# Kernel optimization log

Hardware: AMD Instinct MI355X
Metric: run time of the kernel (lower is better)

Reference implementation:

```python
import jax, jax.numpy as jnp
import numpy as np

H, C = 4, 32          # heads, per-head channels (hidden_dim = 128)
HID = H * C
NC, NM, E, DIN = 100000, 20000, 400000, 64


def _gat_conv(x_src, x_dst, src, dst, Wsrc, Wdst, asrc, adst, bias):
    """PyG-style bipartite GATConv: gather -> leaky-relu attention -> segment softmax -> scatter."""
    n_dst = x_dst.shape[0]
    hs = (x_src @ Wsrc).reshape(-1, H, C)            # [Ns, H, C]
    hd = (x_dst @ Wdst).reshape(-1, H, C)            # [Nd, H, C]
    a_s = jnp.sum(hs * asrc, axis=-1)                # [Ns, H]
    a_d = jnp.sum(hd * adst, axis=-1)                # [Nd, H]
    e = jax.nn.leaky_relu(a_s[src] + a_d[dst], 0.2)  # [E, H]
    m = jax.ops.segment_max(e, dst, num_segments=n_dst)
    m = jnp.where(jnp.isfinite(m), m, 0.0)           # isolated dst nodes -> -inf max
    ex = jnp.exp(e - m[dst])
    den = jax.ops.segment_sum(ex, dst, num_segments=n_dst)
    alpha = ex / (den[dst] + 1e-16)                  # per-destination segment softmax
    out = jax.ops.segment_sum(hs[src] * alpha[:, :, None], dst, num_segments=n_dst)
    return out.reshape(n_dst, HID) + bias            # concat heads + bias


def _mlp2(x, W1, b1, W2, b2):
    return jax.nn.relu(x @ W1 + b1) @ W2 + b2


def setup_inputs():
    key = jax.random.key(0)
    ks = iter(jax.random.split(key, 80))
    def rn(shape, s):
        return jax.random.normal(next(ks), shape, dtype=jnp.float32) * s
    inp = {}
    inp['x_card'] = rn((NC, DIN), 1.0)
    inp['x_merchant'] = rn((NM, DIN), 1.0)
    for l, din in ((0, DIN), (1, HID)):
        for et in ('cm', 'mc'):
            p = 'l%d_%s_' % (l, et)
            g = (2.0 / (din + HID)) ** 0.5
            inp[p + 'Wsrc'] = rn((din, HID), g)
            inp[p + 'Wdst'] = rn((din, HID), g)
            inp[p + 'asrc'] = rn((H, C), 0.1)
            inp[p + 'adst'] = rn((H, C), 0.1)
            inp[p + 'b'] = jnp.zeros((HID,), jnp.float32)
    for nt in ('card', 'merchant'):
        inp['attw_' + nt] = rn((HID, 1), 0.05)
        inp['attb_' + nt] = jnp.zeros((1,), jnp.float32)
    for nt in ('card', 'mer'):
        inp['cls_%s_W1' % nt] = rn((HID, HID // 2), 0.05)
        inp['cls_%s_b1' % nt] = jnp.zeros((HID // 2,), jnp.float32)
        inp['cls_%s_W2' % nt] = rn((HID // 2, 2), 0.05)
        inp['cls_%s_b2' % nt] = jnp.zeros((2,), jnp.float32)
    inp['risk_W1'] = rn((HID, HID // 2), 0.05)
    inp['risk_b1'] = jnp.zeros((HID // 2,), jnp.float32)
    inp['risk_W2'] = rn((HID // 2, 1), 0.05)
    inp['risk_b2'] = jnp.zeros((1,), jnp.float32)
    inp['cm_src'] = jax.random.randint(next(ks), (E,), 0, NC, dtype=jnp.int32)
    inp['cm_dst'] = jax.random.randint(next(ks), (E,), 0, NM, dtype=jnp.int32)
    inp['mc_src'] = jax.random.randint(next(ks), (E,), 0, NM, dtype=jnp.int32)
    inp['mc_dst'] = jax.random.randint(next(ks), (E,), 0, NC, dtype=jnp.int32)
    return inp


def reference(x_card, x_merchant,
              l0_cm_Wsrc, l0_cm_Wdst, l0_cm_asrc, l0_cm_adst, l0_cm_b,
              l0_mc_Wsrc, l0_mc_Wdst, l0_mc_asrc, l0_mc_adst, l0_mc_b,
              l1_cm_Wsrc, l1_cm_Wdst, l1_cm_asrc, l1_cm_adst, l1_cm_b,
              l1_mc_Wsrc, l1_mc_Wdst, l1_mc_asrc, l1_mc_adst, l1_mc_b,
              attw_card, attb_card, attw_merchant, attb_merchant,
              cls_card_W1, cls_card_b1, cls_card_W2, cls_card_b2,
              cls_mer_W1, cls_mer_b1, cls_mer_W2, cls_mer_b2,
              risk_W1, risk_b1, risk_W2, risk_b2,
              cm_src, cm_dst, mc_src, mc_dst):
    xc, xm = x_card, x_merchant
    # HeteroConv layer 0 (each dst type receives exactly one edge type, so mean-aggr is identity)
    xm1 = _gat_conv(xc, xm, cm_src, cm_dst, l0_cm_Wsrc, l0_cm_Wdst, l0_cm_asrc, l0_cm_adst, l0_cm_b)
    xc1 = _gat_conv(xm, xc, mc_src, mc_dst, l0_mc_Wsrc, l0_mc_Wdst, l0_mc_asrc, l0_mc_adst, l0_mc_b)
    # HeteroConv layer 1
    xm2 = _gat_conv(xc1, xm1, cm_src, cm_dst, l1_cm_Wsrc, l1_cm_Wdst, l1_cm_asrc, l1_cm_adst, l1_cm_b)
    xc2 = _gat_conv(xm1, xc1, mc_src, mc_dst, l1_mc_Wsrc, l1_mc_Wdst, l1_mc_asrc, l1_mc_adst, l1_mc_b)
    # graph-level attention: softmax over the node dimension (dim=0), then reweight
    xc2 = xc2 * jax.nn.softmax(xc2 @ attw_card + attb_card, axis=0)
    xm2 = xm2 * jax.nn.softmax(xm2 @ attw_merchant + attb_merchant, axis=0)
    pred_c = _mlp2(xc2, cls_card_W1, cls_card_b1, cls_card_W2, cls_card_b2)
    pred_m = _mlp2(xm2, cls_mer_W1, cls_mer_b1, cls_mer_W2, cls_mer_b2)
    risk_c = jax.nn.sigmoid(_mlp2(xc2, risk_W1, risk_b1, risk_W2, risk_b2))[:, 0]
    risk_m = jax.nn.sigmoid(_mlp2(xm2, risk_W1, risk_b1, risk_W2, risk_b2))[:, 0]
    return (xc2, xm2, pred_c, pred_m, risk_c, risk_m)
```

## Files before the change

kernel.cpp:

```cpp
#include <hip/hip_runtime.h>

typedef _Float16 f16;
typedef _Float16 f16x2 __attribute__((ext_vector_type(2)));
typedef _Float16 f16x4 __attribute__((ext_vector_type(4)));
typedef _Float16 f16x8 __attribute__((ext_vector_type(8)));
typedef float floatx4 __attribute__((ext_vector_type(4)));

constexpr int NC = 100000;
constexpr int NM = 20000;
constexpr int NE = 400000;

constexpr int OFF_XM2 = NC * 128;
constexpr int OFF_PC  = OFF_XM2 + NM * 128;
constexpr int OFF_PM  = OFF_PC + NC * 2;
constexpr int OFF_RC  = OFF_PM + NM * 2;
constexpr int OFF_RM  = OFF_RC + NC;

__device__ __forceinline__ int bpermi(int v, int srclane) {
  return __builtin_amdgcn_ds_bpermute(srclane << 2, v);
}
__device__ __forceinline__ float bpermf(float v, int srclane) {
  int r = __builtin_amdgcn_ds_bpermute(srclane << 2, __builtin_bit_cast(int, v));
  return __builtin_bit_cast(float, r);
}

__global__ void __launch_bounds__(256) k_prep(
    int* zero_base, int nzero, int* stats_i,
    const float* W0, const float* a0, float* v0,
    const float* W1, const float* a1, float* v1,
    const float* W2, const float* a2, float* v2,
    const float* W3, const float* a3, float* v3,
    const float* cb1, const float* mb1, const float* rb1, float* bC, float* bM,
    const float* S0, const float* S1, const float* S2, const float* S3,
    const float* c1, const float* m1, const float* r1,
    f16* BfL0cm, f16* BfL0mc, f16* BfL1cm, f16* BfL1mc, f16* BfC, f16* BfM) {
  int b = blockIdx.x, t = threadIdx.x;
  if (b < 256) {
    for (int i = b * 256 + t; i < nzero + 4; i += 256 * 256) {
      if (i < nzero) zero_base[i] = 0; else stats_i[i - nzero] = 0;
    }
  } else if (b == 256) {
    const float* Wd[4] = {W0, W1, W2, W3};
    const float* ad[4] = {a0, a1, a2, a3};
    float* vd[4] = {v0, v1, v2, v3};
    for (int idx = t; idx < 1536; idx += 256) {
      int mat, base;
      if (idx < 256)       { mat = 0; base = 0; }
      else if (idx < 512)  { mat = 1; base = 256; }
      else if (idx < 1024) { mat = 2; base = 512; }
      else                 { mat = 3; base = 1024; }
      int local = idx - base, k = local >> 2, h = local & 3;
      const float* W = Wd[mat]; const float* a = ad[mat];
      float s = 0.f;
      for (int c = 0; c < 32; ++c) s += W[k * 128 + h * 32 + c] * a[h * 32 + c];
      vd[mat][local] = s;
    }
    if (t < 128) {
      bC[t] = (t < 64) ? cb1[t] : rb1[t - 64];
      bM[t] = (t < 64) ? mb1[t] : rb1[t - 64];
    }
  } else {
    int s = b - 257;
    const float* Wp = nullptr; const float* cA = nullptr; const float* cB = nullptr;
    f16* dst; int kt;
    if (s < 2)       { Wp = S0; dst = BfL0cm; kt = s; }
    else if (s < 4)  { Wp = S1; dst = BfL0mc; kt = s - 2; }
    else if (s < 8)  { Wp = S2; dst = BfL1cm; kt = s - 4; }
    else if (s < 12) { Wp = S3; dst = BfL1mc; kt = s - 8; }
    else if (s < 16) { cA = c1; cB = r1; dst = BfC; kt = s - 12; }
    else             { cA = m1; cB = r1; dst = BfM; kt = s - 16; }
    for (int e = t; e < 512; e += 256) {
      int lane = e & 63, ct = e >> 6;
      int m = lane & 15, q = lane >> 4;
      int col = ct * 16 + m;
      f16x8 frag;
      #pragma unroll
      for (int j = 0; j < 8; ++j) {
        int k = kt * 32 + q * 8 + j;
        float val = Wp ? Wp[k * 128 + col]
                       : (col < 64 ? cA[k * 64 + col] : cB[k * 64 + (col - 64)]);
        frag[j] = (f16)val;
      }
      *reinterpret_cast<f16x8*>(&dst[(size_t)((kt * 8 + ct) * 64 + lane) * 8]) = frag;
    }
  }
}

__global__ void k_hist(const int* cm_dst, const int* mc_dst,
                       int* cnt_cm, int* cnt_mc, int* rank_cm, int* rank_mc) {
  int i = blockIdx.x * blockDim.x + threadIdx.x;
  if (i < NE) {
    rank_cm[i] = atomicAdd(&cnt_cm[cm_dst[i]], 1);
    rank_mc[i] = atomicAdd(&cnt_mc[mc_dst[i]], 1);
  }
}

__global__ void __launch_bounds__(256) k_scan1(const int* cnt_cm, const int* cnt_mc,
                                               int* offs_cm, int* offs_mc, int* parts) {
  int b = blockIdx.x;
  const int* cnt; int* offs; int n, chunk;
  if (b < 20) { cnt = cnt_cm; offs = offs_cm; n = NM; chunk = b; }
  else        { cnt = cnt_mc; offs = offs_mc; n = NC; chunk = b - 20; }
  int t = threadIdx.x;
  int base = chunk * 1024;
  int v[4]; int tsum = 0;
  #pragma unroll
  for (int j = 0; j < 4; ++j) {
    int idx = base + t * 4 + j;
    v[j] = (idx < n) ? cnt[idx] : 0;
    tsum += v[j];
  }
  __shared__ int sd[256];
  sd[t] = tsum; __syncthreads();
  for (int off = 1; off < 256; off <<= 1) {
    int x = (t >= off) ? sd[t - off] : 0;
    __syncthreads();
    sd[t] += x;
    __syncthreads();
  }
  int excl = sd[t] - tsum;
  int r = excl;
  #pragma unroll
  for (int j = 0; j < 4; ++j) {
    int idx = base + t * 4 + j;
    if (idx < n) offs[idx] = r;
    r += v[j];
  }
  if (t == 0) parts[b] = sd[255];
}

__global__ void __launch_bounds__(256) k_scan2(int* parts) {
  int b = blockIdx.x;
  int base = (b == 0) ? 0 : 20;
  int n = (b == 0) ? 20 : 98;
  int t = threadIdx.x;
  __shared__ int sd[128];
  int v = 0;
  if (t < 128) { v = (t < n) ? parts[base + t] : 0; sd[t] = v; }
  __syncthreads();
  for (int off = 1; off < 128; off <<= 1) {
    int x = 0;
    if (t < 128 && t >= off) x = sd[t - off];
    __syncthreads();
    if (t < 128) sd[t] += x;
    __syncthreads();
  }
  if (t < 128 && t < n) parts[base + t] = sd[t] - v;
}

__global__ void k_scan3(int* offs_cm, int* offs_mc, const int* parts) {
  int i = blockIdx.x * blockDim.x + threadIdx.x;
  if (i < NM) {
    offs_cm[i] += parts[i >> 10];
  } else if (i < NM + NC) {
    int j = i - NM;
    offs_mc[j] += parts[20 + (j >> 10)];
  }
  if (i == 0) { offs_cm[NM] = NE; offs_mc[NC] = NE; }
}

__global__ void k_scatter(const int* cm_src, const int* cm_dst,
                          const int* mc_src, const int* mc_dst,
                          const int* rank_cm, const int* rank_mc,
                          const int* offs_cm, const int* offs_mc,
                          int* csr_cm, int* csr_mc) {
  int i = blockIdx.x * blockDim.x + threadIdx.x;
  if (i < NE) {
    int p = offs_cm[cm_dst[i]] + rank_cm[i];
    csr_cm[p] = cm_src[i];
    int q = offs_mc[mc_dst[i]] + rank_mc[i];
    csr_mc[q] = mc_src[i];
  }
}

struct GemmSide {
  const float* x; const f16* Bf;
  const float* asrc; const float* v; f16* hs; float* asO; float* adO;
  const float* bias; const float* wnum; const float* den; float* outx;
  const float* W2; const float* B2; const float* w2r; const float* b2r;
  float* pred; float* risk;
  int M;
};

template<int K, int EPI>
__global__ void __launch_bounds__(256) k_gemm(GemmSide A, GemmSide B, int gridA) {
  constexpr int PP = K + 8;
  constexpr int F4 = K / 4;
  __shared__ f16 xs16[64 * PP];
  const bool isA = (int)blockIdx.x < gridA;
  GemmSide S = isA ? A : B;
  const int blk = isA ? (int)blockIdx.x : (int)blockIdx.x - gridA;
  const int rows0 = blk * 64;
  const int t = (int)threadIdx.x;
  float invden_s = 0.f;
  if constexpr (EPI == 1) invden_s = 1.0f / S.den[0];
  const float4* x4 = reinterpret_cast<const float4*>(S.x);
  #pragma unroll
  for (int ii = 0; ii < (64 * F4) / 256; ++ii) {
    int idx = t + ii * 256;
    int r = idx / F4, f = idx % F4;
    int gr = rows0 + r;
    float4 val = {0.f, 0.f, 0.f, 0.f};
    if (gr < S.M) val = x4[(size_t)gr * F4 + f];
    f16x4 hv; hv.x = (f16)val.x; hv.y = (f16)val.y; hv.z = (f16)val.z; hv.w = (f16)val.w;
    *reinterpret_cast<f16x4*>(&xs16[r * PP + f * 4]) = hv;
    if constexpr (EPI == 1) {
      if (gr < S.M) {
        float w = S.wnum[gr] * invden_s;
        float4 ov = {val.x * w, val.y * w, val.z * w, val.w * w};
        *reinterpret_cast<float4*>(&S.outx[(size_t)gr * 128 + f * 4]) = ov;
      }
    }
  }
  __syncthreads();
  const int lane = t & 63, w = t >> 6;
  const int m = lane & 15, q = lane >> 4;
  const int rbase = w * 16;
  floatx4 acc[8];
  #pragma unroll
  for (int ct = 0; ct < 8; ++ct) acc[ct] = {0.f, 0.f, 0.f, 0.f};
  const f16x8* Bf8 = reinterpret_cast<const f16x8*>(S.Bf);
  #pragma unroll
  for (int kt = 0; kt < K / 32; ++kt) {
    f16x8 a = *reinterpret_cast<const f16x8*>(&xs16[(rbase + m) * PP + kt * 32 + q * 8]);
    #pragma unroll
    for (int ct = 0; ct < 8; ++ct) {
      f16x8 b = Bf8[(kt * 8 + ct) * 64 + lane];
      acc[ct] = __builtin_amdgcn_mfma_f32_16x16x32_f16(a, b, acc[ct], 0, 0, 0);
    }
  }
  if constexpr (EPI == 0) {
    #pragma unroll
    for (int reg = 0; reg < 4; ++reg) {
      int gr = rows0 + rbase + q * 4 + reg;
      bool ok = gr < S.M;
      #pragma unroll
      for (int cp = 0; cp < 4; ++cp) {
        float v0 = acc[2 * cp][reg], v1 = acc[2 * cp + 1][reg];
        float w0 = __shfl_xor(v0, 1), w1 = __shfl_xor(v1, 1);
        bool even = (m & 1) == 0;
        f16x2 pr;
        pr.x = (f16)(even ? v0 : w1);
        pr.y = (f16)(even ? w0 : v1);
        int col = even ? (2 * cp) * 16 + m : (2 * cp + 1) * 16 + m - 1;
        if (ok) *reinterpret_cast<f16x2*>(&S.hs[(size_t)gr * 128 + col]) = pr;
      }
    }
    float as0[4], as1[4];
    #pragma unroll
    for (int h = 0; h < 4; ++h) { as0[h] = S.asrc[h * 32 + m]; as1[h] = S.asrc[h * 32 + 16 + m]; }
    #pragma unroll
    for (int reg = 0; reg < 4; ++reg) {
      float p[4];
      #pragma unroll
      for (int h = 0; h < 4; ++h)
        p[h] = acc[2 * h][reg] * as0[h] + acc[2 * h + 1][reg] * as1[h];
      #pragma unroll
      for (int off = 1; off < 16; off <<= 1) {
        #pragma unroll
        for (int h = 0; h < 4; ++h) p[h] += __shfl_xor(p[h], off);
      }
      int gr = rows0 + rbase + q * 4 + reg;
      if (m == 0 && gr < S.M) {
        float4 pv = {p[0], p[1], p[2], p[3]};
        *reinterpret_cast<float4*>(&S.asO[gr * 4]) = pv;
      }
    }
    float qd[4] = {0.f, 0.f, 0.f, 0.f};
    const float4* v4p = reinterpret_cast<const float4*>(S.v);
    constexpr int KS = K / 4;
    #pragma unroll
    for (int i = 0; i < KS; ++i) {
      int k = q * KS + i;
      float xv = (float)xs16[(rbase + m) * PP + k];
      float4 vk = v4p[k];
      qd[0] += xv * vk.x; qd[1] += xv * vk.y; qd[2] += xv * vk.z; qd[3] += xv * vk.w;
    }
    #pragma unroll
    for (int h = 0; h < 4; ++h) {
      qd[h] += __shfl_xor(qd[h], 16);
      qd[h] += __shfl_xor(qd[h], 32);
    }
    int gr2 = rows0 + rbase + m;
    if (q == 0 && gr2 < S.M) {
      float4 qv = {qd[0], qd[1], qd[2], qd[3]};
      *reinterpret_cast<float4*>(&S.adO[gr2 * 4]) = qv;
    }
  } else {
    float wn[4];
    #pragma unroll
    for (int reg = 0; reg < 4; ++reg) {
      int gr = rows0 + rbase + q * 4 + reg;
      wn[reg] = (gr < S.M) ? S.wnum[gr] * invden_s : 0.f;
    }
    float bct[8], w2c0[4], w2c1[4], w2rv[4];
    #pragma unroll
    for (int ct = 0; ct < 8; ++ct) bct[ct] = S.bias[ct * 16 + m];
    #pragma unroll
    for (int ct = 0; ct < 4; ++ct) {
      int col = ct * 16 + m;
      w2c0[ct] = S.W2[col * 2];
      w2c1[ct] = S.W2[col * 2 + 1];
      w2rv[ct] = S.w2r[col];
    }
    #pragma unroll
    for (int reg = 0; reg < 4; ++reg) {
      float p0 = 0.f, p1 = 0.f, rr = 0.f;
      #pragma unroll
      for (int ct = 0; ct < 4; ++ct) {
        float hv = fmaxf(acc[ct][reg] * wn[reg] + bct[ct], 0.f);
        p0 += hv * w2c0[ct];
        p1 += hv * w2c1[ct];
      }
      #pragma unroll
      for (int ct = 4; ct < 8; ++ct) {
        float hv = fmaxf(acc[ct][reg] * wn[reg] + bct[ct], 0.f);
        rr += hv * w2rv[ct - 4];
      }
      #pragma unroll
      for (int off = 1; off < 16; off <<= 1) {
        p0 += __shfl_xor(p0, off);
        p1 += __shfl_xor(p1, off);
        rr += __shfl_xor(rr, off);
      }
      int gr = rows0 + rbase + q * 4 + reg;
      if (m == 0 && gr < S.M) {
        float2 pp = {p0 + S.B2[0], p1 + S.B2[1]};
        *reinterpret_cast<float2*>(&S.pred[gr * 2]) = pp;
        float z = rr + S.b2r[0];
        S.risk[gr] = 1.f / (1.f + __expf(-z));
      }
    }
  }
}

struct AggSide {
  const int* offs; const int* csr; const float* as_; const float* ad;
  const f16* hs; const float* bias; float* out;
  const float* attw; const float* attb; float* logv;
};

__global__ void __launch_bounds__(256) k_agg(AggSide A, AggSide B,
                                             int ndstA, int ndstB, int nwaves) {
  const int wid = (int)blockIdx.x * 4 + ((int)threadIdx.x >> 6);
  if (wid >= nwaves) return;
  const int lane = (int)threadIdx.x & 63;
  if (wid < ndstA) {
    const AggSide S = A;
    const int d = wid;
    const int we = lane >> 2, wh = lane & 3;
    const int ep = lane >> 5;
    const int c4 = lane & 31;
    const int gh = c4 >> 3;
    const int c8 = c4 << 3;
    const int wh4 = wh << 2;
    const int beg = __builtin_amdgcn_readfirstlane(S.offs[d]);
    const int end = __builtin_amdgcn_readfirstlane(S.offs[d + 1]);
    const float adv = S.ad[d * 4 + wh];
    const char* __restrict__ hsb = (const char*)S.hs;
    const char* __restrict__ asb = (const char*)S.as_;
    float m_run = -1e30f, den = 0.f;
    float acc0 = 0.f, acc1 = 0.f, acc2 = 0.f, acc3 = 0.f;
    for (int base = beg; base < end; base += 16) {
      const int n = min(16, end - base);
      int sb = 0; float e = -1e30f;
      if (we < n) {
        int s = S.csr[base + we];
        sb = s << 8;
        float asv = *reinterpret_cast<const float*>(asb + (unsigned)((s << 4) + wh4));
        float ev = asv + adv;
        e = (ev > 0.f) ? ev : 0.2f * ev;
      }
      float cm = e;
      cm = fmaxf(cm, __shfl_xor(cm, 4));
      cm = fmaxf(cm, __shfl_xor(cm, 8));
      if (n > 4) cm = fmaxf(cm, __shfl_xor(cm, 16));
      if (n > 8) cm = fmaxf(cm, __shfl_xor(cm, 32));
      const float m_new = fmaxf(m_run, cm);
      const float scale = __expf(m_run - m_new);
      const float w = __expf(e - m_new);
      float ws = w;
      ws += __shfl_xor(ws, 4);
      ws += __shfl_xor(ws, 8);
      if (n > 4) ws += __shfl_xor(ws, 16);
      if (n > 8) ws += __shfl_xor(ws, 32);
      den = den * scale + ws;
      m_run = m_new;
      const float sg = bpermf(scale, gh);
      acc0 *= sg; acc1 *= sg; acc2 *= sg; acc3 *= sg;
      int j = 0;
      for (; j + 8 <= n; j += 8) {
        int i0 = (j + ep) << 2, i1 = (j + 2 + ep) << 2;
        int i2 = (j + 4 + ep) << 2, i3 = (j + 6 + ep) << 2;
        int s0 = bpermi(sb, i0);
        int s1 = bpermi(sb, i1);
        int s2 = bpermi(sb, i2);
        int s3 = bpermi(sb, i3);
        f16x4 h0 = *reinterpret_cast<const f16x4*>(hsb + (unsigned)(s0 + c8));
        f16x4 h1 = *reinterpret_cast<const f16x4*>(hsb + (unsigned)(s1 + c8));
        f16x4 h2 = *reinterpret_cast<const f16x4*>(hsb + (unsigned)(s2 + c8));
        f16x4 h3 = *reinterpret_cast<const f16x4*>(hsb + (unsigned)(s3 + c8));
        float w0 = bpermf(w, i0 + gh);
        float w1 = bpermf(w, i1 + gh);
        float w2 = bpermf(w, i2 + gh);
        float w3 = bpermf(w, i3 + gh);
        acc0 += w0 * (float)h0.x; acc1 += w0 * (float)h0.y;
        acc2 += w0 * (float)h0.z; acc3 += w0 * (float)h0.w;
        acc0 += w1 * (float)h1.x; acc1 += w1 * (float)h1.y;
        acc2 += w1 * (float)h1.z; acc3 += w1 * (float)h1.w;
        acc0 += w2 * (float)h2.x; acc1 += w2 * (float)h2.y;
        acc2 += w2 * (float)h2.z; acc3 += w2 * (float)h2.w;
        acc0 += w3 * (float)h3.x; acc1 += w3 * (float)h3.y;
        acc2 += w3 * (float)h3.z; acc3 += w3 * (float)h3.w;
      }
      for (; j + 4 <= n; j += 4) {
        int i0 = (j + ep) << 2, i1 = (j + 2 + ep) << 2;
        int s0 = bpermi(sb, i0);
        int s1 = bpermi(sb, i1);
        f16x4 h0 = *reinterpret_cast<const f16x4*>(hsb + (unsigned)(s0 + c8));
        f16x4 h1 = *reinterpret_cast<const f16x4*>(hsb + (unsigned)(s1 + c8));
        float w0 = bpermf(w, i0 + gh);
        float w1 = bpermf(w, i1 + gh);
        acc0 += w0 * (float)h0.x; acc1 += w0 * (float)h0.y;
        acc2 += w0 * (float)h0.z; acc3 += w0 * (float)h0.w;
        acc0 += w1 * (float)h1.x; acc1 += w1 * (float)h1.y;
        acc2 += w1 * (float)h1.z; acc3 += w1 * (float)h1.w;
      }
      for (; j < n; j += 2) {
        int i0 = (j + ep) << 2;
        int s0 = bpermi(sb, i0);
        f16x4 h0 = *reinterpret_cast<const f16x4*>(hsb + (unsigned)(s0 + c8));
        float w0 = bpermf(w, i0 + gh);
        acc0 += w0 * (float)h0.x; acc1 += w0 * (float)h0.y;
        acc2 += w0 * (float)h0.z; acc3 += w0 * (float)h0.w;
      }
    }
    acc0 += __shfl_xor(acc0, 32);
    acc1 += __shfl_xor(acc1, 32);
    acc2 += __shfl_xor(acc2, 32);
    acc3 += __shfl_xor(acc3, 32);
    const float deng = bpermf(den, gh);
    const float invden = (deng > 0.f) ? 1.f / deng : 0.f;
    const float4 b4 = *reinterpret_cast<const float4*>(&S.bias[c4 * 4]);
    float o0 = acc0 * invden + b4.x;
    float o1 = acc1 * invden + b4.y;
    float o2 = acc2 * invden + b4.z;
    float o3 = acc3 * invden + b4.w;
    if (ep == 0) {
      float4 o = {o0, o1, o2, o3};
      *reinterpret_cast<float4*>(&S.out[d * 128 + c4 * 4]) = o;
    }
    if (S.attw) {
      const float4 aw = *reinterpret_cast<const float4*>(&S.attw[c4 * 4]);
      float sl = o0 * aw.x + o1 * aw.y + o2 * aw.z + o3 * aw.w;
      sl += __shfl_xor(sl, 1);
      sl += __shfl_xor(sl, 2);
      sl += __shfl_xor(sl, 4);
      sl += __shfl_xor(sl, 8);
      sl += __shfl_xor(sl, 16);
      if (lane == 0) S.logv[d] = sl + S.attb[0];
    }
  } else {
    const AggSide S = B;
    const int p = wid - ndstA;
    const int half32 = lane & 32;
    const int l5 = lane & 31;
    int d = p * 2 + (lane >> 5);
    const bool dok = d < ndstB;
    if (!dok) d = ndstB - 1;
    const int we = l5 >> 2, wh = l5 & 3;
    const int gh = l5 >> 3;
    const int c8 = l5 << 3;
    const char* __restrict__ hsb = (const char*)S.hs;
    const char* __restrict__ asb = (const char*)S.as_;
    const int beg = S.offs[d];
    const int end = dok ? S.offs[d + 1] : beg;
    const float adv = S.ad[d * 4 + wh];
    int nch = (end - beg + 7) >> 3;
    int nco = __shfl_xor(nch, 32);
    const int ncmax = __builtin_amdgcn_readfirstlane(max(nch, nco));
    float m_run = -1e30f, den = 0.f;
    float acc0 = 0.f, acc1 = 0.f, acc2 = 0.f, acc3 = 0.f;
    for (int cc = 0; cc < ncmax; ++cc) {
      const int n = min(end - beg - cc * 8, 8);
      int sb = 0; float e = -1e30f;
      const bool wv = we < n;
      if (wv) {
        int s = S.csr[beg + cc * 8 + we];
        sb = s << 8;
        float asv = *reinterpret_cast<const float*>(asb + (unsigned)((s << 4) + (wh << 2)));
        float ev = asv + adv;
        e = (ev > 0.f) ? ev : 0.2f * ev;
      }
      float cm = e;
      cm = fmaxf(cm, __shfl_xor(cm, 4));
      cm = fmaxf(cm, __shfl_xor(cm, 8));
      cm = fmaxf(cm, __shfl_xor(cm, 16));
      const float m_new = fmaxf(m_run, cm);
      const float scale = __expf(m_run - m_new);
      const float w = wv ? __expf(e - m_new) : 0.f;
      float ws = w;
      ws += __shfl_xor(ws, 4);
      ws += __shfl_xor(ws, 8);
      ws += __shfl_xor(ws, 16);
      den = den * scale + ws;
      m_run = m_new;
      acc0 *= scale; acc1 *= scale; acc2 *= scale; acc3 *= scale;
      int jv = max(n, 0);
      int jo = __shfl_xor(jv, 32);
      const int jm = __builtin_amdgcn_readfirstlane(max(jv, jo));
      int j = 0;
      for (; j + 4 <= jm; j += 4) {
        int i0 = half32 + j * 4, i1 = i0 + 4, i2 = i0 + 8, i3 = i0 + 12;
        int s0 = bpermi(sb, i0);
        int s1 = bpermi(sb, i1);
        int s2 = bpermi(sb, i2);
        int s3 = bpermi(sb, i3);
        f16x4 h0 = *reinterpret_cast<const f16x4*>(hsb + (unsigned)(s0 + c8));
        f16x4 h1 = *reinterpret_cast<const f16x4*>(hsb + (unsigned)(s1 + c8));
        f16x4 h2 = *reinterpret_cast<const f16x4*>(hsb + (unsigned)(s2 + c8));
        f16x4 h3 = *reinterpret_cast<const f16x4*>(hsb + (unsigned)(s3 + c8));
        float w0 = bpermf(w, i0 + gh);
        float w1 = bpermf(w, i1 + gh);
        float w2 = bpermf(w, i2 + gh);
        float w3 = bpermf(w, i3 + gh);
        acc0 += w0 * (float)h0.x; acc1 += w0 * (float)h0.y;
        acc2 += w0 * (float)h0.z; acc3 += w0 * (float)h0.w;
        acc0 += w1 * (float)h1.x; acc1 += w1 * (float)h1.y;
        acc2 += w1 * (float)h1.z; acc3 += w1 * (float)h1.w;
        acc0 += w2 * (float)h2.x; acc1 += w2 * (float)h2.y;
        acc2 += w2 * (float)h2.z; acc3 += w2 * (float)h2.w;
        acc0 += w3 * (float)h3.x; acc1 += w3 * (float)h3.y;
        acc2 += w3 * (float)h3.z; acc3 += w3 * (float)h3.w;
      }
      for (; j < jm; ++j) {
        int i0 = half32 + j * 4;
        int s0 = bpermi(sb, i0);
        f16x4 h0 = *reinterpret_cast<const f16x4*>(hsb + (unsigned)(s0 + c8));
        float w0 = bpermf(w, i0 + gh);
        acc0 += w0 * (float)h0.x; acc1 += w0 * (float)h0.y;
        acc2 += w0 * (float)h0.z; acc3 += w0 * (float)h0.w;
      }
    }
    const float invden = (den > 0.f) ? 1.f / den : 0.f;
    const float4 b4 = *reinterpret_cast<const float4*>(&S.bias[l5 * 4]);
    float o0 = acc0 * invden + b4.x;
    float o1 = acc1 * invden + b4.y;
    float o2 = acc2 * invden + b4.z;
    float o3 = acc3 * invden + b4.w;
    if (dok) {
      float4 o = {o0, o1, o2, o3};
      *reinterpret_cast<float4*>(&S.out[d * 128 + l5 * 4]) = o;
    }
    if (S.attw) {
      const float4 aw = *reinterpret_cast<const float4*>(&S.attw[l5 * 4]);
      float sl = o0 * aw.x + o1 * aw.y + o2 * aw.z + o3 * aw.w;
      sl += __shfl_xor(sl, 1);
      sl += __shfl_xor(sl, 2);
      sl += __shfl_xor(sl, 4);
      sl += __shfl_xor(sl, 8);
      sl += __shfl_xor(sl, 16);
      if (l5 == 0 && dok) S.logv[d] = sl + S.attb[0];
    }
  }
}

__global__ void __launch_bounds__(1024) k_stats(const float* logc, const float* logm, float* stats) {
  const float* src = (blockIdx.x == 0) ? logc : logm;
  int n = (blockIdx.x == 0) ? NC : NM;
  float m = -1e30f;
  for (int i = threadIdx.x; i < n; i += 1024) m = fmaxf(m, src[i]);
  __shared__ float sd[1024];
  sd[threadIdx.x] = m; __syncthreads();
  for (int off = 512; off > 0; off >>= 1) {
    if ((int)threadIdx.x < off) sd[threadIdx.x] = fmaxf(sd[threadIdx.x], sd[threadIdx.x + off]);
    __syncthreads();
  }
  if (threadIdx.x == 0) stats[blockIdx.x] = sd[0];
}

__global__ void __launch_bounds__(256) k_expsum(float* logc, float* logm, float* stats) {
  bool card = (int)blockIdx.x < 256;
  float* logv = card ? logc : logm;
  int n = card ? NC : NM;
  float mx = card ? stats[0] : stats[1];
  int b0 = card ? (int)blockIdx.x : (int)blockIdx.x - 256;
  int nb = card ? 256 : 64;
  float local = 0.f;
  for (int i = b0 * 256 + (int)threadIdx.x; i < n; i += nb * 256) {
    float e = __expf(logv[i] - mx);
    logv[i] = e;
    local += e;
  }
  __shared__ float sd[256];
  sd[threadIdx.x] = local; __syncthreads();
  for (int off = 128; off > 0; off >>= 1) {
    if ((int)threadIdx.x < off) sd[threadIdx.x] += sd[threadIdx.x + off];
    __syncthreads();
  }
  if (threadIdx.x == 0) atomicAdd(card ? &stats[2] : &stats[3], sd[0]);
}

extern "C" void kernel_launch(void* const* d_in, const int* in_sizes, int n_in,
                              void* d_out, int out_size, void* d_ws, size_t ws_size,
                              hipStream_t stream) {
  (void)in_sizes; (void)n_in; (void)out_size; (void)ws_size;
  const float* x_card    = (const float*)d_in[0];
  const float* x_mer     = (const float*)d_in[1];
  const float* l0cm_Wsrc = (const float*)d_in[2];
  const float* l0cm_Wdst = (const float*)d_in[3];
  const float* l0cm_asrc = (const float*)d_in[4];
  const float* l0cm_adst = (const float*)d_in[5];
  const float* l0cm_b    = (const float*)d_in[6];
  const float* l0mc_Wsrc = (const float*)d_in[7];
  const float* l0mc_Wdst = (const float*)d_in[8];
  const float* l0mc_asrc = (const float*)d_in[9];
  const float* l0mc_adst = (const float*)d_in[10];
  const float* l0mc_b    = (const float*)d_in[11];
  const float* l1cm_Wsrc = (const float*)d_in[12];
  const float* l1cm_Wdst = (const float*)d_in[13];
  const float* l1cm_asrc = (const float*)d_in[14];
  const float* l1cm_adst = (const float*)d_in[15];
  const float* l1cm_b    = (const float*)d_in[16];
  const float* l1mc_Wsrc = (const float*)d_in[17];
  const float* l1mc_Wdst = (const float*)d_in[18];
  const float* l1mc_asrc = (const float*)d_in[19];
  const float* l1mc_adst = (const float*)d_in[20];
  const float* l1mc_b    = (const float*)d_in[21];
  const float* attw_c    = (const float*)d_in[22];
  const float* attb_c    = (const float*)d_in[23];
  const float* attw_m    = (const float*)d_in[24];
  const float* attb_m    = (const float*)d_in[25];
  const float* clsc_W1   = (const float*)d_in[26];
  const float* clsc_b1   = (const float*)d_in[27];
  const float* clsc_W2   = (const float*)d_in[28];
  const float* clsc_b2   = (const float*)d_in[29];
  const float* clsm_W1   = (const float*)d_in[30];
  const float* clsm_b1   = (const float*)d_in[31];
  const float* clsm_W2   = (const float*)d_in[32];
  const float* clsm_b2   = (const float*)d_in[33];
  const float* risk_W1   = (const float*)d_in[34];
  const float* risk_b1   = (const float*)d_in[35];
  const float* risk_W2   = (const float*)d_in[36];
  const float* risk_b2   = (const float*)d_in[37];
  const int*   cm_src    = (const int*)d_in[38];
  const int*   cm_dst    = (const int*)d_in[39];
  const int*   mc_src    = (const int*)d_in[40];
  const int*   mc_dst    = (const int*)d_in[41];
  float* out = (float*)d_out;

  float* base = (float*)d_ws;
  size_t o = 0;
  auto alloc = [&](size_t n) { float* p = base + o; o += (n + 3) & ~size_t(3); return p; };
  float* hs_card = alloc((size_t)NC * 128);
  float* xc1     = alloc((size_t)NC * 128);
  float* hs_mer  = alloc((size_t)NM * 128);
  float* xm1     = alloc((size_t)NM * 128);
  float* as_card = alloc((size_t)NC * 4);
  float* ad_card = alloc((size_t)NC * 4);
  float* as_mer  = alloc((size_t)NM * 4);
  float* ad_mer  = alloc((size_t)NM * 4);
  float* v_l0cm  = alloc(512);
  float* v_l0mc  = alloc(512);
  float* v_l1cm  = alloc(512);
  float* v_l1mc  = alloc(512);
  float* bC      = alloc(128);
  float* bM      = alloc(128);
  f16* Bf_l0cm = (f16*)alloc(64 * 128 / 2);
  f16* Bf_l0mc = (f16*)alloc(64 * 128 / 2);
  f16* Bf_l1cm = (f16*)alloc(128 * 128 / 2);
  f16* Bf_l1mc = (f16*)alloc(128 * 128 / 2);
  f16* Bf_catC = (f16*)alloc(128 * 128 / 2);
  f16* Bf_catM = (f16*)alloc(128 * 128 / 2);
  float* logc    = alloc(NC);
  float* logm    = alloc(NM);
  float* stats   = alloc(4);
  int* cnt_cm  = (int*)alloc(NM);
  int* cnt_mc  = (int*)alloc(NC);
  int* offs_cm = (int*)alloc(NM + 1);
  int* offs_mc = (int*)alloc(NC + 1);
  int* parts   = (int*)alloc(128);
  int* csr_cm  = (int*)alloc(NE);
  int* csr_mc  = (int*)alloc(NE);
  int* rank_cm = (int*)alloc(NE);
  int* rank_mc = (int*)alloc(NE);

  const dim3 B256(256);
  k_prep<<<dim3(277), B256, 0, stream>>>(
      cnt_cm, NM + NC, (int*)stats,
      l0cm_Wdst, l0cm_adst, v_l0cm, l0mc_Wdst, l0mc_adst, v_l0mc,
      l1cm_Wdst, l1cm_adst, v_l1cm, l1mc_Wdst, l1mc_adst, v_l1mc,
      clsc_b1, clsm_b1, risk_b1, bC, bM,
      l0cm_Wsrc, l0mc_Wsrc, l1cm_Wsrc, l1mc_Wsrc,
      clsc_W1, clsm_W1, risk_W1,
      Bf_l0cm, Bf_l0mc, Bf_l1cm, Bf_l1mc, Bf_catC, Bf_catM);
  const int gEdge = (NE + 255) / 256;
  k_hist<<<dim3(gEdge), B256, 0, stream>>>(cm_dst, mc_dst, cnt_cm, cnt_mc,
                                           rank_cm, rank_mc);
  k_scan1<<<dim3(118), B256, 0, stream>>>(cnt_cm, cnt_mc, offs_cm, offs_mc, parts);
  k_scan2<<<dim3(2), B256, 0, stream>>>(parts);
  k_scan3<<<dim3(469), B256, 0, stream>>>(offs_cm, offs_mc, parts);
  k_scatter<<<dim3(gEdge), B256, 0, stream>>>(cm_src, cm_dst, mc_src, mc_dst,
                                              rank_cm, rank_mc, offs_cm, offs_mc,
                                              csr_cm, csr_mc);
  const int gA = (NC + 63) / 64;
  const int gB = (NM + 63) / 64;
  const int NWAVES = NM + (NC + 1) / 2;
  const int gAgg = (NWAVES + 3) / 4;

  GemmSide sA, sB;
  AggSide aA, aB;
  sA = {x_card, Bf_l0cm, l0cm_asrc, v_l0mc, (f16*)hs_card, as_card, ad_card,
        nullptr, nullptr, nullptr, nullptr, nullptr, nullptr, nullptr, nullptr,
        nullptr, nullptr, NC};
  sB = {x_mer, Bf_l0mc, l0mc_asrc, v_l0cm, (f16*)hs_mer, as_mer, ad_mer,
        nullptr, nullptr, nullptr, nullptr, nullptr, nullptr, nullptr, nullptr,
        nullptr, nullptr, NM};
  k_gemm<64, 0><<<dim3(gA + gB), B256, 0, stream>>>(sA, sB, gA);
  aA = {offs_cm, csr_cm, as_card, ad_mer, (const f16*)hs_card, l0cm_b, xm1,
        nullptr, nullptr, nullptr};
  aB = {offs_mc, csr_mc, as_mer, ad_card, (const f16*)hs_mer, l0mc_b, xc1,
        nullptr, nullptr, nullptr};
  k_agg<<<dim3(gAgg), B256, 0, stream>>>(aA, aB, NM, NC, NWAVES);
  sA = {xc1, Bf_l1cm, l1cm_asrc, v_l1mc, (f16*)hs_card, as_card, ad_card,
        nullptr, nullptr, nullptr, nullptr, nullptr, nullptr, nullptr, nullptr,
        nullptr, nullptr, NC};
  sB = {xm1, Bf_l1mc, l1mc_asrc, v_l1cm, (f16*)hs_mer, as_mer, ad_mer,
        nullptr, nullptr, nullptr, nullptr, nullptr, nullptr, nullptr, nullptr,
        nullptr, nullptr, NM};
  k_gemm<128, 0><<<dim3(gA + gB), B256, 0, stream>>>(sA, sB, gA);
  aA = {offs_cm, csr_cm, as_card, ad_mer, (const f16*)hs_card, l1cm_b, xm1,
        attw_m, attb_m, logm};
  aB = {offs_mc, csr_mc, as_mer, ad_card, (const f16*)hs_mer, l1mc_b, xc1,
        attw_c, attb_c, logc};
  k_agg<<<dim3(gAgg), B256, 0, stream>>>(aA, aB, NM, NC, NWAVES);
  k_stats<<<dim3(2), dim3(1024), 0, stream>>>(logc, logm, stats);
  k_expsum<<<dim3(320), B256, 0, stream>>>(logc, logm, stats);
  sA = {xc1, Bf_catC, nullptr, nullptr, nullptr, nullptr, nullptr,
        bC, logc, stats + 2, out,
        clsc_W2, clsc_b2, risk_W2, risk_b2,
        out + OFF_PC, out + OFF_RC, NC};
  sB = {xm1, Bf_catM, nullptr, nullptr, nullptr, nullptr, nullptr,
        bM, logm, stats + 3, out + OFF_XM2,
        clsm_W2, clsm_b2, risk_W2, risk_b2,
        out + OFF_PM, out + OFF_RM, NM};
  k_gemm<128, 1><<<dim3(gA + gB), B256, 0, stream>>>(sA, sB, gA);
}
```

Before: 447.3 us.

## Fuse histogram into prep, scatter into first GEMM, parallelize max reduction

The edge histogram moves into the prep kernel, and zeroing of the count arrays moves to a hipMemsetAsync. The CSR scatter runs as extra blocks appended to the first GEMM launch. The two-block max reduction becomes a 320-block reduction that combines results with an atomicMax on order-preserving unsigned float keys. The intent is to cut the number of kernel launches and the serial tail of the stats reduction, at the cost of a wider GEMM grid and atomics on the stats words.

```diff
diff --git a/kernel.cpp b/kernel.cpp
--- a/kernel.cpp
+++ b/kernel.cpp
@@ -23,9 +23,17 @@
   int r = __builtin_amdgcn_ds_bpermute(srclane << 2, __builtin_bit_cast(int, v));
   return __builtin_bit_cast(float, r);
 }
+__device__ __forceinline__ unsigned fkey(float f) {
+  unsigned u = __builtin_bit_cast(unsigned, f);
+  return (u >> 31) ? ~u : (u | 0x80000000u);
+}
+__device__ __forceinline__ float fdec(unsigned k) {
+  unsigned u = (k >> 31) ? (k ^ 0x80000000u) : ~k;
+  return __builtin_bit_cast(float, u);
+}
 
 __global__ void __launch_bounds__(256) k_prep(
-    int* zero_base, int nzero, int* stats_i,
+    int* stats_i,
     const float* W0, const float* a0, float* v0,
     const float* W1, const float* a1, float* v1,
     const float* W2, const float* a2, float* v2,
@@ -33,13 +41,11 @@
     const float* cb1, const float* mb1, const float* rb1, float* bC, float* bM,
     const float* S0, const float* S1, const float* S2, const float* S3,
     const float* c1, const float* m1, const float* r1,
-    f16* BfL0cm, f16* BfL0mc, f16* BfL1cm, f16* BfL1mc, f16* BfC, f16* BfM) {
+    f16* BfL0cm, f16* BfL0mc, f16* BfL1cm, f16* BfL1mc, f16* BfC, f16* BfM,
+    const int* cm_dst, const int* mc_dst, int* cnt_cm, int* cnt_mc,
+    int* rank_cm, int* rank_mc) {
   int b = blockIdx.x, t = threadIdx.x;
-  if (b < 256) {
-    for (int i = b * 256 + t; i < nzero + 4; i += 256 * 256) {
-      if (i < nzero) zero_base[i] = 0; else stats_i[i - nzero] = 0;
-    }
-  } else if (b == 256) {
+  if (b == 0) {
     const float* Wd[4] = {W0, W1, W2, W3};
     const float* ad[4] = {a0, a1, a2, a3};
     float* vd[4] = {v0, v1, v2, v3};
@@ -59,8 +65,9 @@
       bC[t] = (t < 64) ? cb1[t] : rb1[t - 64];
       bM[t] = (t < 64) ? mb1[t] : rb1[t - 64];
     }
-  } else {
-    int s = b - 257;
+    if (t < 4) stats_i[t] = 0;
+  } else if (b <= 20) {
+    int s = b - 1;
     const float* Wp = nullptr; const float* cA = nullptr; const float* cB = nullptr;
     f16* dst; int kt;
     if (s < 2)       { Wp = S0; dst = BfL0cm; kt = s; }
@@ -83,15 +90,12 @@
       }
       *reinterpret_cast<f16x8*>(&dst[(size_t)((kt * 8 + ct) * 64 + lane) * 8]) = frag;
     }
-  }
-}
-
-__global__ void k_hist(const int* cm_dst, const int* mc_dst,
-                       int* cnt_cm, int* cnt_mc, int* rank_cm, int* rank_mc) {
-  int i = blockIdx.x * blockDim.x + threadIdx.x;
-  if (i < NE) {
-    rank_cm[i] = atomicAdd(&cnt_cm[cm_dst[i]], 1);
-    rank_mc[i] = atomicAdd(&cnt_mc[mc_dst[i]], 1);
+  } else {
+    int i = (b - 21) * 256 + t;
+    if (i < NE) {
+      rank_cm[i] = atomicAdd(&cnt_cm[cm_dst[i]], 1);
+      rank_mc[i] = atomicAdd(&cnt_mc[mc_dst[i]], 1);
+    }
   }
 }
 
@@ -159,20 +163,6 @@
   if (i == 0) { offs_cm[NM] = NE; offs_mc[NC] = NE; }
 }
 
-__global__ void k_scatter(const int* cm_src, const int* cm_dst,
-                          const int* mc_src, const int* mc_dst,
-                          const int* rank_cm, const int* rank_mc,
-                          const int* offs_cm, const int* offs_mc,
-                          int* csr_cm, int* csr_mc) {
-  int i = blockIdx.x * blockDim.x + threadIdx.x;
-  if (i < NE) {
-    int p = offs_cm[cm_dst[i]] + rank_cm[i];
-    csr_cm[p] = cm_src[i];
-    int q = offs_mc[mc_dst[i]] + rank_mc[i];
-    csr_mc[q] = mc_src[i];
-  }
-}
-
 struct GemmSide {
   const float* x; const f16* Bf;
   const float* asrc; const float* v; f16* hs; float* asO; float* adO;
@@ -182,8 +172,27 @@
   int M;
 };
 
+struct ScatPack {
+  const int* cm_src; const int* cm_dst; const int* mc_src; const int* mc_dst;
+  const int* rank_cm; const int* rank_mc; const int* offs_cm; const int* offs_mc;
+  int* csr_cm; int* csr_mc;
+};
+
 template<int K, int EPI>
-__global__ void __launch_bounds__(256) k_gemm(GemmSide A, GemmSide B, int gridA) {
+__global__ void __launch_bounds__(256) k_gemm(GemmSide A, GemmSide B, int gridA,
+                                              int nGemm, ScatPack sp) {
+  if constexpr (K == 64 && EPI == 0) {
+    if ((int)blockIdx.x >= nGemm) {
+      int i = ((int)blockIdx.x - nGemm) * 256 + (int)threadIdx.x;
+      if (i < NE) {
+        int p = sp.offs_cm[sp.cm_dst[i]] + sp.rank_cm[i];
+        sp.csr_cm[p] = sp.cm_src[i];
+        int q = sp.offs_mc[sp.mc_dst[i]] + sp.rank_mc[i];
+        sp.csr_mc[q] = sp.mc_src[i];
+      }
+      return;
+    }
+  }
   constexpr int PP = K + 8;
   constexpr int F4 = K / 4;
   __shared__ f16 xs16[64 * PP];
@@ -565,25 +574,32 @@
   }
 }
 
-__global__ void __launch_bounds__(1024) k_stats(const float* logc, const float* logm, float* stats) {
-  const float* src = (blockIdx.x == 0) ? logc : logm;
-  int n = (blockIdx.x == 0) ? NC : NM;
+__global__ void __launch_bounds__(256) k_stats(const float* logc, const float* logm,
+                                               unsigned* statsu) {
+  bool card = (int)blockIdx.x < 256;
+  const float* src = card ? logc : logm;
+  int n = card ? NC : NM;
+  int b0 = card ? (int)blockIdx.x : (int)blockIdx.x - 256;
+  int nb = card ? 256 : 64;
   float m = -1e30f;
-  for (int i = threadIdx.x; i < n; i += 1024) m = fmaxf(m, src[i]);
-  __shared__ float sd[1024];
-  sd[threadIdx.x] = m; __syncthreads();
-  for (int off = 512; off > 0; off >>= 1) {
-    if ((int)threadIdx.x < off) sd[threadIdx.x] = fmaxf(sd[threadIdx.x], sd[threadIdx.x + off]);
-    __syncthreads();
-  }
-  if (threadIdx.x == 0) stats[blockIdx.x] = sd[0];
+  for (int i = b0 * 256 + (int)threadIdx.x; i < n; i += nb * 256) m = fmaxf(m, src[i]);
+  #pragma unroll
+  for (int off = 1; off < 64; off <<= 1) m = fmaxf(m, __shfl_xor(m, off));
+  __shared__ float sm[4];
+  if (((int)threadIdx.x & 63) == 0) sm[threadIdx.x >> 6] = m;
+  __syncthreads();
+  if (threadIdx.x == 0) {
+    float mm = fmaxf(fmaxf(sm[0], sm[1]), fmaxf(sm[2], sm[3]));
+    atomicMax(statsu + (card ? 0 : 1), fkey(mm));
+  }
 }
 
 __global__ void __launch_bounds__(256) k_expsum(float* logc, float* logm, float* stats) {
   bool card = (int)blockIdx.x < 256;
   float* logv = card ? logc : logm;
   int n = card ? NC : NM;
-  float mx = card ? stats[0] : stats[1];
+  const unsigned* statsu = (const unsigned*)stats;
+  float mx = fdec(card ? statsu[0] : statsu[1]);
   int b0 = card ? (int)blockIdx.x : (int)blockIdx.x - 256;
   int nb = card ? 256 : 64;
   float local = 0.f;
@@ -686,23 +702,21 @@
   int* rank_mc = (int*)alloc(NE);
 
   const dim3 B256(256);
-  k_prep<<<dim3(277), B256, 0, stream>>>(
-      cnt_cm, NM + NC, (int*)stats,
+  const int gEdge = (NE + 255) / 256;
+  hipMemsetAsync(cnt_cm, 0, (size_t)(NM + NC) * sizeof(int), stream);
+  k_prep<<<dim3(21 + gEdge), B256, 0, stream>>>(
+      (int*)stats,
       l0cm_Wdst, l0cm_adst, v_l0cm, l0mc_Wdst, l0mc_adst, v_l0mc,
       l1cm_Wdst, l1cm_adst, v_l1cm, l1mc_Wdst, l1mc_adst, v_l1mc,
       clsc_b1, clsm_b1, risk_b1, bC, bM,
       l0cm_Wsrc, l0mc_Wsrc, l1cm_Wsrc, l1mc_Wsrc,
       clsc_W1, clsm_W1, risk_W1,
-      Bf_l0cm, Bf_l0mc, Bf_l1cm, Bf_l1mc, Bf_catC, Bf_catM);
-  const int gEdge = (NE + 255) / 256;
-  k_hist<<<dim3(gEdge), B256, 0, stream>>>(cm_dst, mc_dst, cnt_cm, cnt_mc,
-                                           rank_cm, rank_mc);
+      Bf_l0cm, Bf_l0mc, Bf_l1cm, Bf_l1mc, Bf_catC, Bf_catM,
+      cm_dst, mc_dst, cnt_cm, cnt_mc, rank_cm, rank_mc);
   k_scan1<<<dim3(118), B256, 0, stream>>>(cnt_cm, cnt_mc, offs_cm, offs_mc, parts);
   k_scan2<<<dim3(2), B256, 0, stream>>>(parts);
   k_scan3<<<dim3(469), B256, 0, stream>>>(offs_cm, offs_mc, parts);
-  k_scatter<<<dim3(gEdge), B256, 0, stream>>>(cm_src, cm_dst, mc_src, mc_dst,
-                                              rank_cm, rank_mc, offs_cm, offs_mc,
-                                              csr_cm, csr_mc);
+
   const int gA = (NC + 63) / 64;
   const int gB = (NM + 63) / 64;
   const int NWAVES = NM + (NC + 1) / 2;
@@ -710,13 +724,16 @@
 
   GemmSide sA, sB;
   AggSide aA, aB;
+  ScatPack sp = {cm_src, cm_dst, mc_src, mc_dst,
+                 rank_cm, rank_mc, offs_cm, offs_mc, csr_cm, csr_mc};
+  ScatPack spNull = {};
   sA = {x_card, Bf_l0cm, l0cm_asrc, v_l0mc, (f16*)hs_card, as_card, ad_card,
         nullptr, nullptr, nullptr, nullptr, nullptr, nullptr, nullptr, nullptr,
         nullptr, nullptr, NC};
   sB = {x_mer, Bf_l0mc, l0mc_asrc, v_l0cm, (f16*)hs_mer, as_mer, ad_mer,
         nullptr, nullptr, nullptr, nullptr, nullptr, nullptr, nullptr, nullptr,
         nullptr, nullptr, NM};
-  k_gemm<64, 0><<<dim3(gA + gB), B256, 0, stream>>>(sA, sB, gA);
+  k_gemm<64, 0><<<dim3(gA + gB + gEdge), B256, 0, stream>>>(sA, sB, gA, gA + gB, sp);
   aA = {offs_cm, csr_cm, as_card, ad_mer, (const f16*)hs_card, l0cm_b, xm1,
         nullptr, nullptr, nullptr};
   aB = {offs_mc, csr_mc, as_mer, ad_card, (const f16*)hs_mer, l0mc_b, xc1,
@@ -728,13 +745,13 @@
   sB = {xm1, Bf_l1mc, l1mc_asrc, v_l1cm, (f16*)hs_mer, as_mer, ad_mer,
         nullptr, nullptr, nullptr, nullptr, nullptr, nullptr, nullptr, nullptr,
         nullptr, nullptr, NM};
-  k_gemm<128, 0><<<dim3(gA + gB), B256, 0, stream>>>(sA, sB, gA);
+  k_gemm<128, 0><<<dim3(gA + gB), B256, 0, stream>>>(sA, sB, gA, gA + gB, spNull);
   aA = {offs_cm, csr_cm, as_card, ad_mer, (const f16*)hs_card, l1cm_b, xm1,
         attw_m, attb_m, logm};
   aB = {offs_mc, csr_mc, as_mer, ad_card, (const f16*)hs_mer, l1mc_b, xc1,
         attw_c, attb_c, logc};
   k_agg<<<dim3(gAgg), B256, 0, stream>>>(aA, aB, NM, NC, NWAVES);
-  k_stats<<<dim3(2), dim3(1024), 0, stream>>>(logc, logm, stats);
+  k_stats<<<dim3(320), B256, 0, stream>>>(logc, logm, (unsigned*)stats);
   k_expsum<<<dim3(320), B256, 0, stream>>>(logc, logm, stats);
   sA = {xc1, Bf_catC, nullptr, nullptr, nullptr, nullptr, nullptr,
         bC, logc, stats + 2, out,
@@ -744,5 +761,5 @@
         bM, logm, stats + 3, out + OFF_XM2,
         clsm_W2, clsm_b2, risk_W2, risk_b2,
         out + OFF_PM, out + OFF_RM, NM};
-  k_gemm<128, 1><<<dim3(gA + gB), B256, 0, stream>>>(sA, sB, gA);
-}
+  k_gemm<128, 1><<<dim3(gA + gB), B256, 0, stream>>>(sA, sB, gA, gA + gB, spNull);
+}
```

After: 422.1 us. 5.6% less time.
